# Optimization experiments

Measured on AMD Instinct MI355X. Metric: run time of the kernel, lower is better.

## Reference

```python
import jax, jax.numpy as jnp
import numpy as np

N_NODES = 50000
N_EDGES = 800000
D = 128          # node/edge feature dim
H = 128          # MLP hidden dim
T_EDGE = 3       # number of edge types
T_NODE = 2       # number of node types


def setup_inputs() -> dict:
    key = jax.random.key(0)
    ks = jax.random.split(key, 14)
    s = 0.05  # weight init scale
    return {
        "nf": jax.random.normal(ks[0], (N_NODES, D), jnp.float32),
        "ef": jax.random.normal(ks[1], (N_EDGES, D), jnp.float32),
        "src": jax.random.randint(ks[2], (N_EDGES,), 0, N_NODES, jnp.int32),
        "dst": jax.random.randint(ks[3], (N_EDGES,), 0, N_NODES, jnp.int32),
        "etype": jax.random.randint(ks[4], (N_EDGES,), 0, T_EDGE, jnp.int32),
        "ntype": jax.random.randint(ks[5], (N_NODES,), 0, T_NODE, jnp.int32),
        # per-edge-type MLP: Linear(3D->H), ReLU, Linear(H->D)
        "We_h": jax.random.normal(ks[6], (T_EDGE, 3 * D, H), jnp.float32) * s,
        "be_h": jnp.zeros((T_EDGE, H), jnp.float32),
        "We_o": jax.random.normal(ks[7], (T_EDGE, H, D), jnp.float32) * s,
        "be_o": jnp.zeros((T_EDGE, D), jnp.float32),
        # per-node-type MLP: Linear(2D->H), ReLU, Linear(H->D)
        "Wn_h": jax.random.normal(ks[8], (T_NODE, 2 * D, H), jnp.float32) * s,
        "bn_h": jnp.zeros((T_NODE, H), jnp.float32),
        "Wn_o": jax.random.normal(ks[9], (T_NODE, H, D), jnp.float32) * s,
        "bn_o": jnp.zeros((T_NODE, D), jnp.float32),
    }


def _typed_mlp(x, tvec, Wh, bh, Wo, bo):
    """Per-type 2-layer MLP dispatch, then the source's gather-back.

    The torch code builds type_pos_list (stable concat of per-type index lists,
    i.e. a stable argsort of tvec) and then indexes the concatenated per-type
    outputs with that same permutation (`updated[type_perm]`, a gather rather
    than an inverse-permutation scatter). We reproduce that exactly:
    out_final[j] = out_correct[perm[perm[j]]].
    """
    T = Wh.shape[0]
    out = jnp.zeros((x.shape[0], Wo.shape[-1]), x.dtype)
    for k in range(T):  # small fixed number of types
        y = jax.nn.relu(x @ Wh[k] + bh[k]) @ Wo[k] + bo[k]
        out = jnp.where((tvec == k)[:, None], y, out)
    perm = jnp.argsort(tvec)  # jax argsort is stable
    return out[perm[perm]]


def reference(nf, ef, src, dst, etype, ntype,
              We_h, be_h, We_o, be_o, Wn_h, bn_h, Wn_o, bn_o):
    # edge update: cat([ef, src_nf, dst_nf]) -> per-type MLP
    em_in = jnp.concatenate([ef, nf[src], nf[dst]], axis=-1)  # [E, 3D]
    new_ef = _typed_mlp(em_in, etype, We_h, be_h, We_o, be_o)  # [E, D]
    # message passing: copy_e('h') messages, sum reduce into dst nodes
    agg_m = jax.ops.segment_sum(new_ef, dst, num_segments=nf.shape[0])  # [N, D]
    # node update: cat([agg_m, nf]) -> per-type MLP
    nm_in = jnp.concatenate([agg_m, nf], axis=-1)  # [N, 2D]
    new_nf = _typed_mlp(nm_in, ntype, Wn_h, bn_h, Wn_o, bn_o)  # [N, D]
    return new_nf, new_ef
```

## Files before the change

kernel.cpp:

```cpp
#include <hip/hip_runtime.h>

typedef __bf16 bf16_t;
typedef bf16_t bf16x8_t __attribute__((ext_vector_type(8)));
typedef float  f32x4_t  __attribute__((ext_vector_type(4)));

#define RCHUNK 4096

__global__ void pack_w_kernel(const float* __restrict__ W, bf16_t* __restrict__ out,
                              int T, int Ksrc, int k0, int KB)
{
  int total = T * KB * 8 * 512;
  for (int idx = blockIdx.x * blockDim.x + threadIdx.x; idx < total;
       idx += gridDim.x * blockDim.x) {
    int j  = idx & 7;
    int l  = (idx >> 3) & 63;
    int nb = (idx >> 9) & 7;
    int r  = idx >> 12;
    int kb = r % KB;
    int t  = r / KB;
    int k = k0 + kb * 32 + ((l >> 4) << 3) + j;
    int n = nb * 16 + (l & 15);
    out[idx] = (bf16_t)W[((size_t)t * Ksrc + k) * 128 + n];
  }
}

template <int T>
__global__ void count_types_kernel(const int* __restrict__ tv, int n,
                                   int* __restrict__ blkcnt)
{
  __shared__ int cnt[T];
  int tid = threadIdx.x, b = blockIdx.x;
  if (tid < T) cnt[tid] = 0;
  __syncthreads();
  int lo = b * RCHUNK, hi = min(n, lo + RCHUNK);
  int loc[T];
#pragma unroll
  for (int t = 0; t < T; ++t) loc[t] = 0;
  for (int i = lo + tid; i < hi; i += 256) {
    int tq = tv[i];
#pragma unroll
    for (int t = 0; t < T; ++t) loc[t] += (tq == t);
  }
#pragma unroll
  for (int t = 0; t < T; ++t)
    if (loc[t]) atomicAdd(&cnt[t], loc[t]);
  __syncthreads();
  if (tid < T) blkcnt[b * T + tid] = cnt[tid];
}

template <int T>
__global__ void scan_blocks_kernel(const int* __restrict__ blkcnt, int nblocks,
                                   int* __restrict__ blkbase)
{
  __shared__ int sh[256];
  __shared__ int tot[T];
  int tid = threadIdx.x;
  int myc[T], excl[T];
#pragma unroll
  for (int t = 0; t < T; ++t) myc[t] = (tid < nblocks) ? blkcnt[tid * T + t] : 0;
#pragma unroll
  for (int t = 0; t < T; ++t) {
    sh[tid] = myc[t];
    __syncthreads();
    for (int off = 1; off < 256; off <<= 1) {
      int v = (tid >= off) ? sh[tid - off] : 0;
      __syncthreads();
      sh[tid] += v;
      __syncthreads();
    }
    excl[t] = sh[tid] - myc[t];
    if (tid == 255) tot[t] = sh[255];
    __syncthreads();
  }
  if (tid < nblocks) {
    int run = 0;
#pragma unroll
    for (int t = 0; t < T; ++t) {
      blkbase[tid * T + t] = run + excl[t];
      run += tot[t];
    }
  }
}

template <int T>
__global__ void write_ranks_kernel(const int* __restrict__ tv, int n,
                                   const int* __restrict__ blkbase,
                                   int* __restrict__ rank, int* __restrict__ perm)
{
  __shared__ int sh[256];
  int tid = threadIdx.x, b = blockIdx.x;
  int lo = b * RCHUNK + tid * 16;
  int tvq[16];
  int myc[T];
#pragma unroll
  for (int t = 0; t < T; ++t) myc[t] = 0;
#pragma unroll
  for (int q = 0; q < 16; ++q) {
    int i = lo + q;
    int tq = (i < n) ? tv[i] : -1;
    tvq[q] = tq;
#pragma unroll
    for (int t = 0; t < T; ++t) myc[t] += (tq == t);
  }
  int mybase[T];
#pragma unroll
  for (int t = 0; t < T; ++t) {
    sh[tid] = myc[t];
    __syncthreads();
    for (int off = 1; off < 256; off <<= 1) {
      int v = (tid >= off) ? sh[tid - off] : 0;
      __syncthreads();
      sh[tid] += v;
      __syncthreads();
    }
    mybase[t] = blkbase[b * T + t] + sh[tid] - myc[t];
    __syncthreads();
  }
#pragma unroll
  for (int q = 0; q < 16; ++q) {
    int tq = tvq[q];
    if (tq < 0) continue;
    int r = 0;
#pragma unroll
    for (int t = 0; t < T; ++t)
      if (tq == t) { r = mybase[t]; mybase[t] = r + 1; }
    rank[lo + q] = r;
    perm[r] = lo + q;
  }
}

__global__ __launch_bounds__(256) void precompute_p_kernel(
    const float* __restrict__ nf,
    const bf16_t* __restrict__ pW1s, const bf16_t* __restrict__ pW1d,
    const bf16_t* __restrict__ pWn1b,
    bf16_t* __restrict__ Ps, bf16_t* __restrict__ Pd, bf16_t* __restrict__ Pn,
    int Nn)
{
  __shared__ char Wsm[32768];
  const int which = blockIdx.x & 7, tile = blockIdx.x >> 3;
  const bf16_t* pB; bf16_t* po;
  if (which < 3)      { pB = pW1s + which * 16384;       po = Ps + (size_t)which * Nn * 128; }
  else if (which < 6) { pB = pW1d + (which - 3) * 16384; po = Pd + (size_t)(which - 3) * Nn * 128; }
  else                { pB = pWn1b + (which - 6) * 16384; po = Pn + (size_t)(which - 6) * Nn * 128; }

  const int tid = threadIdx.x, l = tid & 63, w = tid >> 6;
  const int rb = (w >> 1) * 32, cb = (w & 1) * 64, l15 = l & 15;
  const int koff = (l >> 4) << 3;

  {
    const uint4* g = (const uint4*)pB;
    uint4* d = (uint4*)Wsm;
#pragma unroll
    for (int q = 0; q < 8; ++q) d[q * 256 + tid] = g[q * 256 + tid];
  }

  const int base = tile * 64;
  const int r0 = base + rb + l15, r1 = r0 + 16;
  const float* q0 = nf + (size_t)min(r0, Nn - 1) * 128 + koff;
  const float* q1 = nf + (size_t)min(r1, Nn - 1) * 128 + koff;
  f32x4_t areg[2][4][2];
#pragma unroll
  for (int kb = 0; kb < 4; ++kb) {
    areg[0][kb][0] = ((const f32x4_t*)(q0 + kb * 32))[0];
    areg[0][kb][1] = ((const f32x4_t*)(q0 + kb * 32))[1];
    areg[1][kb][0] = ((const f32x4_t*)(q1 + kb * 32))[0];
    areg[1][kb][1] = ((const f32x4_t*)(q1 + kb * 32))[1];
  }
  __syncthreads();

  f32x4_t acc[2][4];
#pragma unroll
  for (int m = 0; m < 2; ++m)
#pragma unroll
    for (int n = 0; n < 4; ++n) acc[m][n] = (f32x4_t){0.f, 0.f, 0.f, 0.f};

#pragma unroll
  for (int kb = 0; kb < 4; ++kb) {
    bf16x8_t bfr[4];
#pragma unroll
    for (int n = 0; n < 4; ++n)
      bfr[n] = *(const bf16x8_t*)(Wsm + ((kb * 8 + (cb >> 4) + n) * 64 + l) * 16);
    bf16x8_t a0, a1;
#pragma unroll
    for (int z = 0; z < 4; ++z) {
      a0[z] = (bf16_t)areg[0][kb][0][z]; a0[4 + z] = (bf16_t)areg[0][kb][1][z];
      a1[z] = (bf16_t)areg[1][kb][0][z]; a1[4 + z] = (bf16_t)areg[1][kb][1][z];
    }
#pragma unroll
    for (int n = 0; n < 4; ++n) {
      acc[0][n] = __builtin_amdgcn_mfma_f32_16x16x32_bf16(a0, bfr[n], acc[0][n], 0, 0, 0);
      acc[1][n] = __builtin_amdgcn_mfma_f32_16x16x32_bf16(a1, bfr[n], acc[1][n], 0, 0, 0);
    }
  }

#pragma unroll
  for (int n = 0; n < 4; ++n) {
    int col = cb + 16 * n + l15;
#pragma unroll
    for (int m = 0; m < 2; ++m)
#pragma unroll
      for (int jj = 0; jj < 4; ++jj) {
        int row = rb + 16 * m + ((l >> 4) << 2) + jj;
        int node = base + row;
        if (node < Nn) po[(size_t)node * 128 + col] = (bf16_t)acc[m][n][jj];
      }
  }
}

template <bool EDGE>
__global__ __launch_bounds__(256, 2) void mlp3_kernel(
    const float* __restrict__ feat,
    const int* __restrict__ src, const int* __restrict__ dst,
    const int* __restrict__ tvec,
    const int* __restrict__ perm, const int* __restrict__ rank,
    const bf16_t* __restrict__ pW1, const float* __restrict__ b1,
    const bf16_t* __restrict__ pW2, const float* __restrict__ b2,
    const bf16_t* __restrict__ P1, const bf16_t* __restrict__ P2, int pnodes,
    float* __restrict__ out, float* __restrict__ agg_out, int Ntot)
{
  __shared__ char Wsm[32768];
  __shared__ char Psm[16384];
  __shared__ char Hsm[16384];
  __shared__ int sm_e[64], sm_j[64], sm_ty[64];
  __shared__ int sm_s0[64], sm_s1[64], sm_dj[64];
  __shared__ int sm_tmin, sm_tmax;

  const int tid = threadIdx.x;
  const int l = tid & 63, w = tid >> 6;
  const int rb = (w >> 1) * 32, cb = (w & 1) * 64;
  const int l15 = l & 15;
  const int koff = (l >> 4) << 3;

  const int tiles = (Ntot + 63) >> 6;
  const int tpb = (tiles + gridDim.x - 1) / gridDim.x;
  const int tb0 = blockIdx.x * tpb;
  const int tb1 = min(tiles, tb0 + tpb);

  int cur_t = -1;
  bf16x8_t w2r[16];
  float bh[4], bo[4];

  for (int tile = tb0; tile < tb1; ++tile) {
    const int base = tile << 6;
    __syncthreads();
    if (tid < 64) {
      int pos = base + tid;
      int tyv = -1;
      if (pos < Ntot) {
        int e = perm[pos], j = rank[pos];
        sm_e[tid] = e; sm_j[tid] = j;
        tyv = tvec[e];
        if (EDGE) { sm_s0[tid] = src[e]; sm_s1[tid] = dst[e]; sm_dj[tid] = dst[j]; }
      } else {
        sm_e[tid] = 0; sm_j[tid] = -1;
        if (EDGE) { sm_s0[tid] = 0; sm_s1[tid] = 0; sm_dj[tid] = 0; }
      }
      sm_ty[tid] = tyv;
      int tmn = tyv < 0 ? 99 : tyv, tmx = tyv;
#pragma unroll
      for (int off = 32; off >= 1; off >>= 1) {
        tmn = min(tmn, __shfl_xor(tmn, off));
        tmx = max(tmx, __shfl_xor(tmx, off));
      }
      if (tid == 0) { sm_tmin = tmn; sm_tmax = tmx < 0 ? 0 : tmx; }
    }
    __syncthreads();

    const int ar0 = rb + l15, ar1 = ar0 + 16;
    const float* q0 = feat + (size_t)sm_e[ar0] * 128 + koff;
    const float* q1 = feat + (size_t)sm_e[ar1] * 128 + koff;
    f32x4_t areg[2][4][2];
#pragma unroll
    for (int kb = 0; kb < 4; ++kb) {
      areg[0][kb][0] = ((const f32x4_t*)(q0 + kb * 32))[0];
      areg[0][kb][1] = ((const f32x4_t*)(q0 + kb * 32))[1];
      areg[1][kb][0] = ((const f32x4_t*)(q1 + kb * 32))[0];
      areg[1][kb][1] = ((const f32x4_t*)(q1 + kb * 32))[1];
    }

#pragma unroll
    for (int q = 0; q < 4; ++q) {
      int idx = tid * 4 + q;
      int row = idx >> 4, c8 = idx & 15;
      int ty = max(sm_ty[row], 0);
      bf16x8_t s;
      if (EDGE) {
        bf16x8_t u = ((const bf16x8_t*)(P1 + ((size_t)ty * pnodes + sm_s0[row]) * 128))[c8];
        bf16x8_t v = ((const bf16x8_t*)(P2 + ((size_t)ty * pnodes + sm_s1[row]) * 128))[c8];
#pragma unroll
        for (int z = 0; z < 8; ++z) s[z] = (bf16_t)((float)u[z] + (float)v[z]);
      } else {
        s = ((const bf16x8_t*)(P1 + ((size_t)ty * pnodes + sm_e[row]) * 128))[c8];
      }
      *(bf16x8_t*)(Psm + row * 256 + ((c8 ^ (row & 15)) << 4)) = s;
    }

    const int tmin = sm_tmin, tmax = sm_tmax;
    for (int t = tmin; t <= tmax; ++t) {
      if (t != cur_t) {
        __syncthreads();
        {
          const uint4* g = (const uint4*)(pW1 + (size_t)t * 16384);
          uint4* d = (uint4*)Wsm;
#pragma unroll
          for (int q = 0; q < 8; ++q) d[q * 256 + tid] = g[q * 256 + tid];
        }
        {
          const bf16x8_t* g2 = (const bf16x8_t*)pW2;
#pragma unroll
          for (int kb = 0; kb < 4; ++kb)
#pragma unroll
            for (int n = 0; n < 4; ++n)
              w2r[kb * 4 + n] = g2[(size_t)((t * 4 + kb) * 8 + (cb >> 4) + n) * 64 + l];
        }
#pragma unroll
        for (int n = 0; n < 4; ++n) {
          bh[n] = b1[t * 128 + cb + 16 * n + l15];
          bo[n] = b2[t * 128 + cb + 16 * n + l15];
        }
        cur_t = t;
        __syncthreads();
      }

      f32x4_t acc[2][4];
#pragma unroll
      for (int m = 0; m < 2; ++m)
#pragma unroll
        for (int n = 0; n < 4; ++n) acc[m][n] = (f32x4_t){0.f, 0.f, 0.f, 0.f};

#pragma unroll
      for (int kb = 0; kb < 4; ++kb) {
        bf16x8_t bfr[4];
#pragma unroll
        for (int n = 0; n < 4; ++n)
          bfr[n] = *(const bf16x8_t*)(Wsm + ((kb * 8 + (cb >> 4) + n) * 64 + l) * 16);
        bf16x8_t a0, a1;
#pragma unroll
        for (int z = 0; z < 4; ++z) {
          a0[z] = (bf16_t)areg[0][kb][0][z]; a0[4 + z] = (bf16_t)areg[0][kb][1][z];
          a1[z] = (bf16_t)areg[1][kb][0][z]; a1[4 + z] = (bf16_t)areg[1][kb][1][z];
        }
#pragma unroll
        for (int n = 0; n < 4; ++n) {
          acc[0][n] = __builtin_amdgcn_mfma_f32_16x16x32_bf16(a0, bfr[n], acc[0][n], 0, 0, 0);
          acc[1][n] = __builtin_amdgcn_mfma_f32_16x16x32_bf16(a1, bfr[n], acc[1][n], 0, 0, 0);
        }
      }

      __syncthreads();
#pragma unroll
      for (int n = 0; n < 4; ++n) {
        int col = cb + 16 * n + l15;
        int byte = col * 2;
#pragma unroll
        for (int m = 0; m < 2; ++m)
#pragma unroll
          for (int jj = 0; jj < 4; ++jj) {
            int row = rb + 16 * m + ((l >> 4) << 2) + jj;
            float pv = (float)*(const bf16_t*)(
                Psm + row * 256 + ((byte & 15) | ((((byte >> 4) ^ (row & 15)) & 15) << 4)));
            float v = acc[m][n][jj] + pv + bh[n];
            v = v > 0.f ? v : 0.f;
            *(bf16_t*)(Hsm + row * 256 + (byte ^ ((row & 7) << 4))) = (bf16_t)v;
          }
      }
      __syncthreads();

      f32x4_t acc2[2][4];
#pragma unroll
      for (int m = 0; m < 2; ++m)
#pragma unroll
        for (int n = 0; n < 4; ++n) acc2[m][n] = (f32x4_t){0.f, 0.f, 0.f, 0.f};

#pragma unroll
      for (int kb = 0; kb < 4; ++kb) {
        int kbyte = kb * 64 + ((l >> 4) << 4);
        int row0 = rb + l15, row1 = row0 + 16;
        bf16x8_t h0 = *(const bf16x8_t*)(Hsm + row0 * 256 + (kbyte ^ ((row0 & 7) << 4)));
        bf16x8_t h1 = *(const bf16x8_t*)(Hsm + row1 * 256 + (kbyte ^ ((row1 & 7) << 4)));
#pragma unroll
        for (int n = 0; n < 4; ++n) {
          acc2[0][n] = __builtin_amdgcn_mfma_f32_16x16x32_bf16(h0, w2r[kb * 4 + n], acc2[0][n], 0, 0, 0);
          acc2[1][n] = __builtin_amdgcn_mfma_f32_16x16x32_bf16(h1, w2r[kb * 4 + n], acc2[1][n], 0, 0, 0);
        }
      }

#pragma unroll
      for (int n = 0; n < 4; ++n) {
        int col = cb + 16 * n + l15;
#pragma unroll
        for (int m = 0; m < 2; ++m)
#pragma unroll
          for (int jj = 0; jj < 4; ++jj) {
            int row = rb + 16 * m + ((l >> 4) << 2) + jj;
            int j = sm_j[row];
            if (j >= 0 && sm_ty[row] == t) {
              float v = acc2[m][n][jj] + bo[n];
              out[(size_t)j * 128 + col] = v;
              if (EDGE)
                unsafeAtomicAdd(agg_out + (size_t)sm_dj[row] * 128 + col, v);
            }
          }
      }
    }
  }
}

extern "C" void kernel_launch(void* const* d_in, const int* in_sizes, int n_in,
                              void* d_out, int out_size, void* d_ws, size_t ws_size,
                              hipStream_t stream)
{
  const float* nf    = (const float*)d_in[0];
  const float* ef    = (const float*)d_in[1];
  const int*   src   = (const int*)d_in[2];
  const int*   dst   = (const int*)d_in[3];
  const int*   etype = (const int*)d_in[4];
  const int*   ntype = (const int*)d_in[5];
  const float* Weh   = (const float*)d_in[6];
  const float* beh   = (const float*)d_in[7];
  const float* Weo   = (const float*)d_in[8];
  const float* beo   = (const float*)d_in[9];
  const float* Wnh   = (const float*)d_in[10];
  const float* bnh   = (const float*)d_in[11];
  const float* Wno   = (const float*)d_in[12];
  const float* bno   = (const float*)d_in[13];

  const int E = in_sizes[2];
  const int N = in_sizes[5];
  const int TE = 3, TN = 2;

  char* ws = (char*)d_ws;
  size_t off = 0;
  auto alloc = [&](size_t bytes) -> char* {
    char* p = ws + off;
    off = (off + bytes + 511) & ~(size_t)511;
    return p;
  };
  bf16_t* pW1e  = (bf16_t*)alloc((size_t)TE * 16384 * 2);
  bf16_t* pW1s  = (bf16_t*)alloc((size_t)TE * 16384 * 2);
  bf16_t* pW1d  = (bf16_t*)alloc((size_t)TE * 16384 * 2);
  bf16_t* pWe2  = (bf16_t*)alloc((size_t)TE * 16384 * 2);
  bf16_t* pWn1a = (bf16_t*)alloc((size_t)TN * 16384 * 2);
  bf16_t* pWn1b = (bf16_t*)alloc((size_t)TN * 16384 * 2);
  bf16_t* pWn2  = (bf16_t*)alloc((size_t)TN * 16384 * 2);
  bf16_t* Ps = (bf16_t*)alloc((size_t)TE * N * 128 * 2);
  bf16_t* Pd = (bf16_t*)alloc((size_t)TE * N * 128 * 2);
  bf16_t* Pn = (bf16_t*)alloc((size_t)TN * N * 128 * 2);
  int* rank_e = (int*)alloc((size_t)E * 4);
  int* perm_e = (int*)alloc((size_t)E * 4);
  int* rank_n = (int*)alloc((size_t)N * 4);
  int* perm_n = (int*)alloc((size_t)N * 4);
  const int NBE = (E + RCHUNK - 1) / RCHUNK;
  const int NBN = (N + RCHUNK - 1) / RCHUNK;
  int* blkcnt_e  = (int*)alloc((size_t)NBE * TE * 4);
  int* blkbase_e = (int*)alloc((size_t)NBE * TE * 4);
  int* blkcnt_n  = (int*)alloc((size_t)NBN * TN * 4);
  int* blkbase_n = (int*)alloc((size_t)NBN * TN * 4);
  float* agg = (float*)alloc((size_t)N * 128 * 4);
  (void)ws_size; (void)n_in; (void)out_size;

  hipMemsetAsync(agg, 0, (size_t)N * 128 * 4, stream);

  pack_w_kernel<<<192, 256, 0, stream>>>(Weh, pW1e, TE, 384, 0, 4);
  pack_w_kernel<<<192, 256, 0, stream>>>(Weh, pW1s, TE, 384, 128, 4);
  pack_w_kernel<<<192, 256, 0, stream>>>(Weh, pW1d, TE, 384, 256, 4);
  pack_w_kernel<<<192, 256, 0, stream>>>(Weo, pWe2, TE, 128, 0, 4);
  pack_w_kernel<<<128, 256, 0, stream>>>(Wnh, pWn1a, TN, 256, 0, 4);
  pack_w_kernel<<<128, 256, 0, stream>>>(Wnh, pWn1b, TN, 256, 128, 4);
  pack_w_kernel<<<128, 256, 0, stream>>>(Wno, pWn2, TN, 128, 0, 4);

  const int ptiles = (N + 63) / 64;
  precompute_p_kernel<<<ptiles * 8, 256, 0, stream>>>(
      nf, pW1s, pW1d, pWn1b, Ps, Pd, Pn, N);

  count_types_kernel<3><<<NBE, 256, 0, stream>>>(etype, E, blkcnt_e);
  scan_blocks_kernel<3><<<1, 256, 0, stream>>>(blkcnt_e, NBE, blkbase_e);
  write_ranks_kernel<3><<<NBE, 256, 0, stream>>>(etype, E, blkbase_e, rank_e, perm_e);

  count_types_kernel<2><<<NBN, 256, 0, stream>>>(ntype, N, blkcnt_n);
  scan_blocks_kernel<2><<<1, 256, 0, stream>>>(blkcnt_n, NBN, blkbase_n);
  write_ranks_kernel<2><<<NBN, 256, 0, stream>>>(ntype, N, blkbase_n, rank_n, perm_n);

  float* out_nf = (float*)d_out;
  float* out_ef = (float*)d_out + (size_t)N * 128;

  mlp3_kernel<true><<<512, 256, 0, stream>>>(
      ef, src, dst, etype, perm_e, rank_e,
      pW1e, beh, pWe2, beo, Ps, Pd, N, out_ef, agg, E);

  mlp3_kernel<false><<<512, 256, 0, stream>>>(
      agg, nullptr, nullptr, ntype, perm_n, rank_n,
      pWn1a, bnh, pWn2, bno, Pn, nullptr, N, out_nf, nullptr, N);
}
```

Before: 833.7 us.

## Replace atomic scatter-add with CSR gather aggregation and type-pure tiles

Aggregation is no longer done with float atomics in the edge MLP epilogue. A destination-sorted CSR (histogram, scan, scatter) is built and a separate kernel gathers new edge features per node. Tiles are also made type-homogeneous using the per-type base offsets, so each tile runs a single MLP pass instead of looping over every type present. In exchange there are several extra small kernels, including a single-block scan, and the output edge features are reread from memory. The summation order also becomes nondeterministic, because the atomic-built edge lists are unordered.

Result: no change. 840.2 us (+0.8%).

```diff
diff --git a/kernel.cpp b/kernel.cpp
--- a/kernel.cpp
+++ b/kernel.cpp
@@ -129,6 +129,87 @@
   }
 }
 
+__global__ void hist_dst_kernel(const int* __restrict__ dst, int E,
+                                int* __restrict__ hist)
+{
+  int i = blockIdx.x * blockDim.x + threadIdx.x;
+  if (i < E) atomicAdd(&hist[dst[i]], 1);
+}
+
+__global__ __launch_bounds__(1024) void scan_offsets_kernel(
+    const int* __restrict__ hist, int n, int* __restrict__ offsets,
+    int* __restrict__ cursor)
+{
+  __shared__ int sh[1024];
+  int tid = threadIdx.x;
+  int per = (n + 1023) >> 10;
+  int lo = tid * per;
+  int s = 0;
+  for (int q = 0; q < per; ++q) {
+    int i = lo + q;
+    if (i < n) s += hist[i];
+  }
+  sh[tid] = s;
+  __syncthreads();
+  for (int off = 1; off < 1024; off <<= 1) {
+    int v = (tid >= off) ? sh[tid - off] : 0;
+    __syncthreads();
+    sh[tid] += v;
+    __syncthreads();
+  }
+  int run = sh[tid] - s;
+  for (int q = 0; q < per; ++q) {
+    int i = lo + q;
+    if (i < n) {
+      offsets[i] = run;
+      cursor[i] = run;
+      run += hist[i];
+    }
+  }
+  if (tid == 1023) offsets[n] = sh[1023];
+}
+
+__global__ void scatter_dst_kernel(const int* __restrict__ dst, int E,
+                                   int* __restrict__ cursor,
+                                   int* __restrict__ edge_by_dst)
+{
+  int i = blockIdx.x * blockDim.x + threadIdx.x;
+  if (i < E) {
+    int pos = atomicAdd(&cursor[dst[i]], 1);
+    edge_by_dst[pos] = i;
+  }
+}
+
+__global__ __launch_bounds__(256) void aggregate_kernel(
+    const float* __restrict__ ef_new, const int* __restrict__ edge_by_dst,
+    const int* __restrict__ offsets, float* __restrict__ agg, int Nn)
+{
+  int gwid = (blockIdx.x * 256 + threadIdx.x) >> 6;
+  int l = threadIdx.x & 63;
+  int nw = (gridDim.x * 256) >> 6;
+  for (int n = gwid; n < Nn; n += nw) {
+    int lo = offsets[n], hi = offsets[n + 1];
+    float sx = 0.f, sy = 0.f;
+    int q = lo;
+    for (; q + 1 < hi; q += 2) {
+      int e0 = edge_by_dst[q], e1 = edge_by_dst[q + 1];
+      float2 v0 = *(const float2*)(ef_new + (size_t)e0 * 128 + l * 2);
+      float2 v1 = *(const float2*)(ef_new + (size_t)e1 * 128 + l * 2);
+      sx += v0.x + v1.x;
+      sy += v0.y + v1.y;
+    }
+    if (q < hi) {
+      int e0 = edge_by_dst[q];
+      float2 v0 = *(const float2*)(ef_new + (size_t)e0 * 128 + l * 2);
+      sx += v0.x;
+      sy += v0.y;
+    }
+    float2 o;
+    o.x = sx; o.y = sy;
+    *(float2*)(agg + (size_t)n * 128 + l * 2) = o;
+  }
+}
+
 __global__ __launch_bounds__(256) void precompute_p_kernel(
     const float* __restrict__ nf,
     const bf16_t* __restrict__ pW1s, const bf16_t* __restrict__ pW1d,
@@ -139,8 +220,8 @@
   __shared__ char Wsm[32768];
   const int which = blockIdx.x & 7, tile = blockIdx.x >> 3;
   const bf16_t* pB; bf16_t* po;
-  if (which < 3)      { pB = pW1s + which * 16384;       po = Ps + (size_t)which * Nn * 128; }
-  else if (which < 6) { pB = pW1d + (which - 3) * 16384; po = Pd + (size_t)(which - 3) * Nn * 128; }
+  if (which < 3)      { pB = pW1s + which * 16384;        po = Ps + (size_t)which * Nn * 128; }
+  else if (which < 6) { pB = pW1d + (which - 3) * 16384;  po = Pd + (size_t)(which - 3) * Nn * 128; }
   else                { pB = pWn1b + (which - 6) * 16384; po = Pn + (size_t)(which - 6) * Nn * 128; }
 
   const int tid = threadIdx.x, l = tid & 63, w = tid >> 6;
@@ -207,23 +288,21 @@
   }
 }
 
-template <bool EDGE>
-__global__ __launch_bounds__(256, 2) void mlp3_kernel(
+template <int T, bool EDGE>
+__global__ __launch_bounds__(256, 2) void mlp4_kernel(
     const float* __restrict__ feat,
     const int* __restrict__ src, const int* __restrict__ dst,
-    const int* __restrict__ tvec,
     const int* __restrict__ perm, const int* __restrict__ rank,
+    const int* __restrict__ tbase,
     const bf16_t* __restrict__ pW1, const float* __restrict__ b1,
     const bf16_t* __restrict__ pW2, const float* __restrict__ b2,
     const bf16_t* __restrict__ P1, const bf16_t* __restrict__ P2, int pnodes,
-    float* __restrict__ out, float* __restrict__ agg_out, int Ntot)
+    float* __restrict__ out, int Ntot)
 {
   __shared__ char Wsm[32768];
   __shared__ char Psm[16384];
   __shared__ char Hsm[16384];
-  __shared__ int sm_e[64], sm_j[64], sm_ty[64];
-  __shared__ int sm_s0[64], sm_s1[64], sm_dj[64];
-  __shared__ int sm_tmin, sm_tmax;
+  __shared__ int sm_e[64], sm_j[64], sm_s0[64], sm_s1[64];
 
   const int tid = threadIdx.x;
   const int l = tid & 63, w = tid >> 6;
@@ -231,38 +310,43 @@
   const int l15 = l & 15;
   const int koff = (l >> 4) << 3;
 
-  const int tiles = (Ntot + 63) >> 6;
-  const int tpb = (tiles + gridDim.x - 1) / gridDim.x;
-  const int tb0 = blockIdx.x * tpb;
-  const int tb1 = min(tiles, tb0 + tpb);
+  const int s0 = tbase[0];
+  const int s1 = (T > 1) ? tbase[1] : Ntot;
+  const int s2 = (T > 2) ? tbase[2] : Ntot;
+  const int e0t = (T > 1) ? s1 : Ntot;
+  const int e1t = (T > 2) ? s2 : Ntot;
+  const int c0 = (e0t - s0 + 63) >> 6;
+  const int c1 = (T > 1) ? ((e1t - s1 + 63) >> 6) : 0;
+  const int c2 = (T > 2) ? ((Ntot - s2 + 63) >> 6) : 0;
+  const int cum1 = c0, cum2 = c0 + c1, total = cum2 + c2;
+
+  const int tpb = (total + gridDim.x - 1) / gridDim.x;
+  const int pt0 = blockIdx.x * tpb;
+  const int pt1 = min(total, pt0 + tpb);
 
   int cur_t = -1;
   bf16x8_t w2r[16];
   float bh[4], bo[4];
 
-  for (int tile = tb0; tile < tb1; ++tile) {
-    const int base = tile << 6;
+  for (int pt = pt0; pt < pt1; ++pt) {
+    const int t = (pt < cum1) ? 0 : ((pt < cum2) ? 1 : 2);
+    const int tstart = (t == 0) ? s0 : ((t == 1) ? s1 : s2);
+    const int tend = (t == 0) ? e0t : ((t == 1) ? e1t : Ntot);
+    const int i = pt - ((t == 0) ? 0 : ((t == 1) ? cum1 : cum2));
+    const int pbase = tstart + (i << 6);
+
     __syncthreads();
     if (tid < 64) {
-      int pos = base + tid;
-      int tyv = -1;
-      if (pos < Ntot) {
-        int e = perm[pos], j = rank[pos];
-        sm_e[tid] = e; sm_j[tid] = j;
-        tyv = tvec[e];
-        if (EDGE) { sm_s0[tid] = src[e]; sm_s1[tid] = dst[e]; sm_dj[tid] = dst[j]; }
+      int pos = pbase + tid;
+      if (pos < tend) {
+        int e = perm[pos];
+        sm_e[tid] = e;
+        sm_j[tid] = rank[pos];
+        if (EDGE) { sm_s0[tid] = src[e]; sm_s1[tid] = dst[e]; }
       } else {
         sm_e[tid] = 0; sm_j[tid] = -1;
-        if (EDGE) { sm_s0[tid] = 0; sm_s1[tid] = 0; sm_dj[tid] = 0; }
-      }
-      sm_ty[tid] = tyv;
-      int tmn = tyv < 0 ? 99 : tyv, tmx = tyv;
-#pragma unroll
-      for (int off = 32; off >= 1; off >>= 1) {
-        tmn = min(tmn, __shfl_xor(tmn, off));
-        tmx = max(tmx, __shfl_xor(tmx, off));
-      }
-      if (tid == 0) { sm_tmin = tmn; sm_tmax = tmx < 0 ? 0 : tmx; }
+        if (EDGE) { sm_s0[tid] = 0; sm_s1[tid] = 0; }
+      }
     }
     __syncthreads();
 
@@ -282,126 +366,117 @@
     for (int q = 0; q < 4; ++q) {
       int idx = tid * 4 + q;
       int row = idx >> 4, c8 = idx & 15;
-      int ty = max(sm_ty[row], 0);
       bf16x8_t s;
       if (EDGE) {
-        bf16x8_t u = ((const bf16x8_t*)(P1 + ((size_t)ty * pnodes + sm_s0[row]) * 128))[c8];
-        bf16x8_t v = ((const bf16x8_t*)(P2 + ((size_t)ty * pnodes + sm_s1[row]) * 128))[c8];
+        bf16x8_t u = ((const bf16x8_t*)(P1 + ((size_t)t * pnodes + sm_s0[row]) * 128))[c8];
+        bf16x8_t v = ((const bf16x8_t*)(P2 + ((size_t)t * pnodes + sm_s1[row]) * 128))[c8];
 #pragma unroll
         for (int z = 0; z < 8; ++z) s[z] = (bf16_t)((float)u[z] + (float)v[z]);
       } else {
-        s = ((const bf16x8_t*)(P1 + ((size_t)ty * pnodes + sm_e[row]) * 128))[c8];
+        s = ((const bf16x8_t*)(P1 + ((size_t)t * pnodes + sm_e[row]) * 128))[c8];
       }
       *(bf16x8_t*)(Psm + row * 256 + ((c8 ^ (row & 15)) << 4)) = s;
     }
 
-    const int tmin = sm_tmin, tmax = sm_tmax;
-    for (int t = tmin; t <= tmax; ++t) {
-      if (t != cur_t) {
-        __syncthreads();
-        {
-          const uint4* g = (const uint4*)(pW1 + (size_t)t * 16384);
-          uint4* d = (uint4*)Wsm;
-#pragma unroll
-          for (int q = 0; q < 8; ++q) d[q * 256 + tid] = g[q * 256 + tid];
+    if (t != cur_t) {
+      __syncthreads();
+      {
+        const uint4* g = (const uint4*)(pW1 + (size_t)t * 16384);
+        uint4* d = (uint4*)Wsm;
+#pragma unroll
+        for (int q = 0; q < 8; ++q) d[q * 256 + tid] = g[q * 256 + tid];
+      }
+      {
+        const bf16x8_t* g2 = (const bf16x8_t*)pW2;
+#pragma unroll
+        for (int kb = 0; kb < 4; ++kb)
+#pragma unroll
+          for (int n = 0; n < 4; ++n)
+            w2r[kb * 4 + n] = g2[(size_t)((t * 4 + kb) * 8 + (cb >> 4) + n) * 64 + l];
+      }
+#pragma unroll
+      for (int n = 0; n < 4; ++n) {
+        bh[n] = b1[t * 128 + cb + 16 * n + l15];
+        bo[n] = b2[t * 128 + cb + 16 * n + l15];
+      }
+      cur_t = t;
+      __syncthreads();
+    }
+
+    f32x4_t acc[2][4];
+#pragma unroll
+    for (int m = 0; m < 2; ++m)
+#pragma unroll
+      for (int n = 0; n < 4; ++n) acc[m][n] = (f32x4_t){0.f, 0.f, 0.f, 0.f};
+
+#pragma unroll
+    for (int kb = 0; kb < 4; ++kb) {
+      bf16x8_t bfr[4];
+#pragma unroll
+      for (int n = 0; n < 4; ++n)
+        bfr[n] = *(const bf16x8_t*)(Wsm + ((kb * 8 + (cb >> 4) + n) * 64 + l) * 16);
+      bf16x8_t a0, a1;
+#pragma unroll
+      for (int z = 0; z < 4; ++z) {
+        a0[z] = (bf16_t)areg[0][kb][0][z]; a0[4 + z] = (bf16_t)areg[0][kb][1][z];
+        a1[z] = (bf16_t)areg[1][kb][0][z]; a1[4 + z] = (bf16_t)areg[1][kb][1][z];
+      }
+#pragma unroll
+      for (int n = 0; n < 4; ++n) {
+        acc[0][n] = __builtin_amdgcn_mfma_f32_16x16x32_bf16(a0, bfr[n], acc[0][n], 0, 0, 0);
+        acc[1][n] = __builtin_amdgcn_mfma_f32_16x16x32_bf16(a1, bfr[n], acc[1][n], 0, 0, 0);
+      }
+    }
+
+    __syncthreads();
+#pragma unroll
+    for (int n = 0; n < 4; ++n) {
+      int col = cb + 16 * n + l15;
+      int byte = col * 2;
+#pragma unroll
+      for (int m = 0; m < 2; ++m)
+#pragma unroll
+        for (int jj = 0; jj < 4; ++jj) {
+          int row = rb + 16 * m + ((l >> 4) << 2) + jj;
+          float pv = (float)*(const bf16_t*)(
+              Psm + row * 256 + ((byte & 15) | ((((byte >> 4) ^ (row & 15)) & 15) << 4)));
+          float v = acc[m][n][jj] + pv + bh[n];
+          v = v > 0.f ? v : 0.f;
+          *(bf16_t*)(Hsm + row * 256 + (byte ^ ((row & 7) << 4))) = (bf16_t)v;
         }
-        {
-          const bf16x8_t* g2 = (const bf16x8_t*)pW2;
-#pragma unroll
-          for (int kb = 0; kb < 4; ++kb)
-#pragma unroll
-            for (int n = 0; n < 4; ++n)
-              w2r[kb * 4 + n] = g2[(size_t)((t * 4 + kb) * 8 + (cb >> 4) + n) * 64 + l];
+    }
+    __syncthreads();
+
+    f32x4_t acc2[2][4];
+#pragma unroll
+    for (int m = 0; m < 2; ++m)
+#pragma unroll
+      for (int n = 0; n < 4; ++n) acc2[m][n] = (f32x4_t){0.f, 0.f, 0.f, 0.f};
+
+#pragma unroll
+    for (int kb = 0; kb < 4; ++kb) {
+      int kbyte = kb * 64 + ((l >> 4) << 4);
+      int row0 = rb + l15, row1 = row0 + 16;
+      bf16x8_t h0 = *(const bf16x8_t*)(Hsm + row0 * 256 + (kbyte ^ ((row0 & 7) << 4)));
+      bf16x8_t h1 = *(const bf16x8_t*)(Hsm + row1 * 256 + (kbyte ^ ((row1 & 7) << 4)));
+#pragma unroll
+      for (int n = 0; n < 4; ++n) {
+        acc2[0][n] = __builtin_amdgcn_mfma_f32_16x16x32_bf16(h0, w2r[kb * 4 + n], acc2[0][n], 0, 0, 0);
+        acc2[1][n] = __builtin_amdgcn_mfma_f32_16x16x32_bf16(h1, w2r[kb * 4 + n], acc2[1][n], 0, 0, 0);
+      }
+    }
+
+#pragma unroll
+    for (int n = 0; n < 4; ++n) {
+      int col = cb + 16 * n + l15;
+#pragma unroll
+      for (int m = 0; m < 2; ++m)
+#pragma unroll
+        for (int jj = 0; jj < 4; ++jj) {
+          int row = rb + 16 * m + ((l >> 4) << 2) + jj;
+          int j = sm_j[row];
+          if (j >= 0) out[(size_t)j * 128 + col] = acc2[m][n][jj] + bo[n];
         }
-#pragma unroll
-        for (int n = 0; n < 4; ++n) {
-          bh[n] = b1[t * 128 + cb + 16 * n + l15];
-          bo[n] = b2[t * 128 + cb + 16 * n + l15];
-        }
-        cur_t = t;
-        __syncthreads();
-      }
-
-      f32x4_t acc[2][4];
-#pragma unroll
-      for (int m = 0; m < 2; ++m)
-#pragma unroll
-        for (int n = 0; n < 4; ++n) acc[m][n] = (f32x4_t){0.f, 0.f, 0.f, 0.f};
-
-#pragma unroll
-      for (int kb = 0; kb < 4; ++kb) {
-        bf16x8_t bfr[4];
-#pragma unroll
-        for (int n = 0; n < 4; ++n)
-          bfr[n] = *(const bf16x8_t*)(Wsm + ((kb * 8 + (cb >> 4) + n) * 64 + l) * 16);
-        bf16x8_t a0, a1;
-#pragma unroll
-        for (int z = 0; z < 4; ++z) {
-          a0[z] = (bf16_t)areg[0][kb][0][z]; a0[4 + z] = (bf16_t)areg[0][kb][1][z];
-          a1[z] = (bf16_t)areg[1][kb][0][z]; a1[4 + z] = (bf16_t)areg[1][kb][1][z];
-        }
-#pragma unroll
-        for (int n = 0; n < 4; ++n) {
-          acc[0][n] = __builtin_amdgcn_mfma_f32_16x16x32_bf16(a0, bfr[n], acc[0][n], 0, 0, 0);
-          acc[1][n] = __builtin_amdgcn_mfma_f32_16x16x32_bf16(a1, bfr[n], acc[1][n], 0, 0, 0);
-        }
-      }
-
-      __syncthreads();
-#pragma unroll
-      for (int n = 0; n < 4; ++n) {
-        int col = cb + 16 * n + l15;
-        int byte = col * 2;
-#pragma unroll
-        for (int m = 0; m < 2; ++m)
-#pragma unroll
-          for (int jj = 0; jj < 4; ++jj) {
-            int row = rb + 16 * m + ((l >> 4) << 2) + jj;
-            float pv = (float)*(const bf16_t*)(
-                Psm + row * 256 + ((byte & 15) | ((((byte >> 4) ^ (row & 15)) & 15) << 4)));
-            float v = acc[m][n][jj] + pv + bh[n];
-            v = v > 0.f ? v : 0.f;
-            *(bf16_t*)(Hsm + row * 256 + (byte ^ ((row & 7) << 4))) = (bf16_t)v;
-          }
-      }
-      __syncthreads();
-
-      f32x4_t acc2[2][4];
-#pragma unroll
-      for (int m = 0; m < 2; ++m)
-#pragma unroll
-        for (int n = 0; n < 4; ++n) acc2[m][n] = (f32x4_t){0.f, 0.f, 0.f, 0.f};
-
-#pragma unroll
-      for (int kb = 0; kb < 4; ++kb) {
-        int kbyte = kb * 64 + ((l >> 4) << 4);
-        int row0 = rb + l15, row1 = row0 + 16;
-        bf16x8_t h0 = *(const bf16x8_t*)(Hsm + row0 * 256 + (kbyte ^ ((row0 & 7) << 4)));
-        bf16x8_t h1 = *(const bf16x8_t*)(Hsm + row1 * 256 + (kbyte ^ ((row1 & 7) << 4)));
-#pragma unroll
-        for (int n = 0; n < 4; ++n) {
-          acc2[0][n] = __builtin_amdgcn_mfma_f32_16x16x32_bf16(h0, w2r[kb * 4 + n], acc2[0][n], 0, 0, 0);
-          acc2[1][n] = __builtin_amdgcn_mfma_f32_16x16x32_bf16(h1, w2r[kb * 4 + n], acc2[1][n], 0, 0, 0);
-        }
-      }
-
-#pragma unroll
-      for (int n = 0; n < 4; ++n) {
-        int col = cb + 16 * n + l15;
-#pragma unroll
-        for (int m = 0; m < 2; ++m)
-#pragma unroll
-          for (int jj = 0; jj < 4; ++jj) {
-            int row = rb + 16 * m + ((l >> 4) << 2) + jj;
-            int j = sm_j[row];
-            if (j >= 0 && sm_ty[row] == t) {
-              float v = acc2[m][n][jj] + bo[n];
-              out[(size_t)j * 128 + col] = v;
-              if (EDGE)
-                unsafeAtomicAdd(agg_out + (size_t)sm_dj[row] * 128 + col, v);
-            }
-          }
-      }
     }
   }
 }
@@ -457,9 +532,11 @@
   int* blkcnt_n  = (int*)alloc((size_t)NBN * TN * 4);
   int* blkbase_n = (int*)alloc((size_t)NBN * TN * 4);
   float* agg = (float*)alloc((size_t)N * 128 * 4);
+  int* dsthist     = (int*)alloc((size_t)N * 4);
+  int* dstoffs     = (int*)alloc((size_t)(N + 1) * 4);
+  int* dstcursor   = (int*)alloc((size_t)N * 4);
+  int* edge_by_dst = (int*)alloc((size_t)E * 4);
   (void)ws_size; (void)n_in; (void)out_size;
-
-  hipMemsetAsync(agg, 0, (size_t)N * 128 * 4, stream);
 
   pack_w_kernel<<<192, 256, 0, stream>>>(Weh, pW1e, TE, 384, 0, 4);
   pack_w_kernel<<<192, 256, 0, stream>>>(Weh, pW1s, TE, 384, 128, 4);
@@ -481,14 +558,21 @@
   scan_blocks_kernel<2><<<1, 256, 0, stream>>>(blkcnt_n, NBN, blkbase_n);
   write_ranks_kernel<2><<<NBN, 256, 0, stream>>>(ntype, N, blkbase_n, rank_n, perm_n);
 
+  hipMemsetAsync(dsthist, 0, (size_t)N * 4, stream);
+  hist_dst_kernel<<<(E + 255) / 256, 256, 0, stream>>>(dst, E, dsthist);
+  scan_offsets_kernel<<<1, 1024, 0, stream>>>(dsthist, N, dstoffs, dstcursor);
+  scatter_dst_kernel<<<(E + 255) / 256, 256, 0, stream>>>(dst, E, dstcursor, edge_by_dst);
+
   float* out_nf = (float*)d_out;
   float* out_ef = (float*)d_out + (size_t)N * 128;
 
-  mlp3_kernel<true><<<512, 256, 0, stream>>>(
-      ef, src, dst, etype, perm_e, rank_e,
-      pW1e, beh, pWe2, beo, Ps, Pd, N, out_ef, agg, E);
-
-  mlp3_kernel<false><<<512, 256, 0, stream>>>(
-      agg, nullptr, nullptr, ntype, perm_n, rank_n,
-      pWn1a, bnh, pWn2, bno, Pn, nullptr, N, out_nf, nullptr, N);
-}
+  mlp4_kernel<3, true><<<512, 256, 0, stream>>>(
+      ef, src, dst, perm_e, rank_e, blkbase_e,
+      pW1e, beh, pWe2, beo, Ps, Pd, N, out_ef, E);
+
+  aggregate_kernel<<<3200, 256, 0, stream>>>(out_ef, edge_by_dst, dstoffs, agg, N);
+
+  mlp4_kernel<2, false><<<512, 256, 0, stream>>>(
+      agg, nullptr, nullptr, perm_n, rank_n, blkbase_n,
+      pWn1a, bnh, pWn2, bno, Pn, nullptr, N, out_nf, N);
+}
```
